# Performance work log

Measured on AMD Instinct MI355X. Metric: run time of the kernel, lower is better.

The kernel has to match this reference:

```python
import jax, jax.numpy as jnp
import numpy as np

B, H, W = 64, 512, 512


def setup_inputs() -> dict:
    key = jax.random.key(0)
    k1, k2 = jax.random.split(key)
    t1 = jax.random.normal(k1, (B, H, W), dtype=jnp.float32)
    t2 = jax.random.normal(k2, (B, H, W), dtype=jnp.float32)
    return {"t1": t1, "t2": t2}


def _wass_p2(a, b):
    # a, b: [H, W] -> flatten to empirical distributions of N values each
    av = a.reshape(-1)
    bv = b.reshape(-1)
    n = av.shape[0]
    a_sorted = jnp.sort(av)
    b_sorted = jnp.sort(bv)
    all_values = jnp.sort(jnp.concatenate([av, bv]))  # [2N]
    deltas = jnp.diff(all_values)                      # [2N-1]
    q = all_values[:-1]
    # right-side searchsorted == count of values <= q  (empirical CDF * N)
    i1 = jnp.searchsorted(a_sorted, q, side="right")
    i2 = jnp.searchsorted(b_sorted, q, side="right")
    c1 = i1.astype(jnp.float32) / n
    c2 = i2.astype(jnp.float32) / n
    # p = 2 branch of the original loss
    return jnp.sqrt(jnp.sum(jnp.square(c1 - c2) * deltas))


def reference(t1, t2):
    losses = jax.vmap(_wass_p2)(t1, t2)  # [B]
    return jnp.mean(losses)
```

## Files before the change

### kernel.cpp

```cpp
#include <hip/hip_runtime.h>
#include <stdint.h>

#define LOG_N   18
#define N_PER   262144
#define BATCHES 64
#define NBINS   4096
#define HALFB   2048
#define HTPB    256
#define SPLITS  16
#define CHUNK   (N_PER / SPLITS)
#define HWORDS  (NBINS / 2)
#define GTPB    512
#define BPT     (NBINS / GTPB)

__device__ __forceinline__ uint32_t f2k(float f) {
    uint32_t u = __float_as_uint(f);
    uint32_t m = (uint32_t)((int32_t)u >> 31) | 0x80000000u;
    return (u ^ m) >> 16;
}
__device__ __forceinline__ uint32_t comp(uint32_t k) {
    bool pos = (k >= 0x8000u);
    int  c   = pos ? ((int)k - 0xB900 + HALFB) : ((int)k - 0x3F00);
    int  lo  = pos ? HALFB : 0;
    int  hi  = lo + HALFB - 1;
    c = c < lo ? lo : c;
    c = c > hi ? hi : c;
    return (uint32_t)c;
}
__device__ __forceinline__ float binEdge(uint32_t c) {
    uint32_t k = (c < HALFB) ? (0x3F00u + c) : (0xB900u + (c - HALFB));
    uint32_t x = k << 16;
    uint32_t u = (x & 0x80000000u) ? (x ^ 0x80000000u) : ~x;
    return __uint_as_float(u);
}

__global__ __launch_bounds__(HTPB) void hist_kernel(
        const float* __restrict__ t1, const float* __restrict__ t2,
        uint32_t* __restrict__ slices) {
    __shared__ uint32_t h[NBINS];
    int tid  = threadIdx.x;
    int tile = blockIdx.x;
    int segL = tile / SPLITS;
    int part = tile % SPLITS;
    int bat  = segL >> 1;
    {
        uint4 z; z.x = z.y = z.z = z.w = 0u;
        uint4* h4 = (uint4*)h;
#pragma unroll
        for (int i = 0; i < 4; ++i) h4[tid + i * HTPB] = z;
    }
    __syncthreads();
    const float4* p = (const float4*)(((segL & 1) ? t2 : t1)
                      + ((size_t)bat << LOG_N) + (size_t)part * CHUNK);
    for (int k = 0; k < 4; ++k) {
        float4 v0 = p[tid + (4 * k + 0) * HTPB];
        float4 v1 = p[tid + (4 * k + 1) * HTPB];
        float4 v2 = p[tid + (4 * k + 2) * HTPB];
        float4 v3 = p[tid + (4 * k + 3) * HTPB];
        atomicAdd(&h[comp(f2k(v0.x))], 1u); atomicAdd(&h[comp(f2k(v0.y))], 1u);
        atomicAdd(&h[comp(f2k(v0.z))], 1u); atomicAdd(&h[comp(f2k(v0.w))], 1u);
        atomicAdd(&h[comp(f2k(v1.x))], 1u); atomicAdd(&h[comp(f2k(v1.y))], 1u);
        atomicAdd(&h[comp(f2k(v1.z))], 1u); atomicAdd(&h[comp(f2k(v1.w))], 1u);
        atomicAdd(&h[comp(f2k(v2.x))], 1u); atomicAdd(&h[comp(f2k(v2.y))], 1u);
        atomicAdd(&h[comp(f2k(v2.z))], 1u); atomicAdd(&h[comp(f2k(v2.w))], 1u);
        atomicAdd(&h[comp(f2k(v3.x))], 1u); atomicAdd(&h[comp(f2k(v3.y))], 1u);
        atomicAdd(&h[comp(f2k(v3.z))], 1u); atomicAdd(&h[comp(f2k(v3.w))], 1u);
    }
    __syncthreads();
    {
        const uint4* h4 = (const uint4*)h;
        uint4* gs4 = (uint4*)(slices + (size_t)tile * HWORDS);
#pragma unroll
        for (int i = tid; i < HWORDS / 4; i += HTPB) {
            uint4 a = h4[2 * i], b = h4[2 * i + 1];
            uint4 o;
            o.x = a.x | (a.y << 16);
            o.y = a.z | (a.w << 16);
            o.z = b.x | (b.y << 16);
            o.w = b.z | (b.w << 16);
            gs4[i] = o;
        }
    }
}

__global__ __launch_bounds__(GTPB) void integ_kernel(
        const uint32_t* __restrict__ slices, double* losses, int ignored) {
    __shared__ short sdiff[NBINS];
    __shared__ int sa[GTPB], sb[GTPB];
    __shared__ double red[GTPB];
    int bl  = blockIdx.x;
    int tid = threadIdx.x;
    const uint32_t* SA = slices + (size_t)(2 * bl) * SPLITS * HWORDS;
    const uint32_t* SB = SA + (size_t)SPLITS * HWORDS;

    for (int w = tid; w < HWORDS; w += GTPB) {
        int d0 = 0, d1 = 0;
#pragma unroll
        for (int s = 0; s < SPLITS; ++s) {
            uint32_t a = SA[s * HWORDS + w];
            uint32_t b = SB[s * HWORDS + w];
            d0 += (int)(a & 0xFFFFu) - (int)(b & 0xFFFFu);
            d1 += (int)(a >> 16)     - (int)(b >> 16);
        }
        sdiff[2 * w]     = (short)d0;
        sdiff[2 * w + 1] = (short)d1;
    }
    __syncthreads();

    int k0 = tid * BPT;
    int diffs[BPT];
    int s = 0;
#pragma unroll
    for (int k = 0; k < BPT; ++k) { int d = sdiff[k0 + k]; diffs[k] = d; s += d; }
    sa[tid] = s;
    __syncthreads();
    int* cur = sa; int* nxt = sb;
    for (int off = 1; off < GTPB; off <<= 1) {
        int v = cur[tid] + ((tid >= off) ? cur[tid - off] : 0);
        nxt[tid] = v;
        __syncthreads();
        int* tmp = cur; cur = nxt; nxt = tmp;
    }
    int D = tid ? cur[tid - 1] : 0;

    double acc = 0.0;
    float vprev = binEdge((uint32_t)k0);
#pragma unroll
    for (int k = 0; k < BPT; ++k) {
        D += diffs[k];
        float vnext = binEdge((uint32_t)(k0 + k + 1));
        if (D) { double dd = (double)D; acc += dd * dd * (double)(vnext - vprev); }
        vprev = vnext;
    }
    red[tid] = acc;
    __syncthreads();
    for (int off = GTPB / 2; off > 0; off >>= 1) {
        if (tid < off) red[tid] += red[tid + off];
        __syncthreads();
    }
    if (tid == 0) {
        const double inv = 1.0 / ((double)N_PER * (double)N_PER);
        losses[bl] = sqrt(red[0] * inv);
    }
}

__global__ void final_kernel(const double* losses, float* out) {
    int tid = threadIdx.x;
    double loss = losses[tid];
    for (int off = 32; off > 0; off >>= 1)
        loss += __shfl_down(loss, off);
    if (tid == 0) out[0] = (float)(loss / (double)BATCHES);
}

extern "C" void kernel_launch(void* const* d_in, const int* in_sizes, int n_in,
                              void* d_out, int out_size, void* d_ws, size_t ws_size,
                              hipStream_t stream) {
    const float* t1 = (const float*)d_in[0];
    const float* t2 = (const float*)d_in[1];
    float* out = (float*)d_out;

    char* ws = (char*)d_ws;
    double*   losses = (double*)ws;
    uint32_t* slices = (uint32_t*)(ws + 1024);
    size_t need = 1024 + (size_t)2 * BATCHES * SPLITS * HWORDS * 4;
    if (ws_size < need) return;

    hipLaunchKernelGGL(hist_kernel, dim3(2 * BATCHES * SPLITS), dim3(HTPB), 0, stream,
                       t1, t2, slices);
    hipLaunchKernelGGL(integ_kernel, dim3(BATCHES), dim3(GTPB), 0, stream,
                       slices, losses, 0);
    hipLaunchKernelGGL(final_kernel, dim3(1), dim3(BATCHES), 0, stream, losses, out);
}
```

Measured before the change: 37.03 us.

## Histogram t1 minus t2 into one signed shared histogram per block

Each histogram block now handles the same chunk of both t1 and t2 with 512 threads, adding +1 for t1 values and -1 for t2 values, so it stores one signed difference histogram instead of two separate ones. This halves the number of slices written and read, and the integration kernel sums the signed 16-bit slices with uint4 loads. The change relies on the per-chunk difference fitting in a signed 16-bit field. It also halves the grid size, which means fewer blocks to hide latency.

```diff
diff --git a/kernel.cpp b/kernel.cpp
--- a/kernel.cpp
+++ b/kernel.cpp
@@ -6,10 +6,10 @@
 #define BATCHES 64
 #define NBINS   4096
 #define HALFB   2048
-#define HTPB    256
+#define HTPB    512
 #define SPLITS  16
 #define CHUNK   (N_PER / SPLITS)
-#define HWORDS  (NBINS / 2)
+#define SLICEW  (NBINS / 2)
 #define GTPB    512
 #define BPT     (NBINS / GTPB)
 
@@ -40,70 +40,85 @@
     __shared__ uint32_t h[NBINS];
     int tid  = threadIdx.x;
     int tile = blockIdx.x;
-    int segL = tile / SPLITS;
+    int bat  = tile / SPLITS;
     int part = tile % SPLITS;
-    int bat  = segL >> 1;
     {
         uint4 z; z.x = z.y = z.z = z.w = 0u;
         uint4* h4 = (uint4*)h;
-#pragma unroll
-        for (int i = 0; i < 4; ++i) h4[tid + i * HTPB] = z;
+        h4[tid] = z; h4[tid + HTPB] = z;
     }
     __syncthreads();
-    const float4* p = (const float4*)(((segL & 1) ? t2 : t1)
-                      + ((size_t)bat << LOG_N) + (size_t)part * CHUNK);
-    for (int k = 0; k < 4; ++k) {
-        float4 v0 = p[tid + (4 * k + 0) * HTPB];
-        float4 v1 = p[tid + (4 * k + 1) * HTPB];
-        float4 v2 = p[tid + (4 * k + 2) * HTPB];
-        float4 v3 = p[tid + (4 * k + 3) * HTPB];
-        atomicAdd(&h[comp(f2k(v0.x))], 1u); atomicAdd(&h[comp(f2k(v0.y))], 1u);
-        atomicAdd(&h[comp(f2k(v0.z))], 1u); atomicAdd(&h[comp(f2k(v0.w))], 1u);
-        atomicAdd(&h[comp(f2k(v1.x))], 1u); atomicAdd(&h[comp(f2k(v1.y))], 1u);
-        atomicAdd(&h[comp(f2k(v1.z))], 1u); atomicAdd(&h[comp(f2k(v1.w))], 1u);
-        atomicAdd(&h[comp(f2k(v2.x))], 1u); atomicAdd(&h[comp(f2k(v2.y))], 1u);
-        atomicAdd(&h[comp(f2k(v2.z))], 1u); atomicAdd(&h[comp(f2k(v2.w))], 1u);
-        atomicAdd(&h[comp(f2k(v3.x))], 1u); atomicAdd(&h[comp(f2k(v3.y))], 1u);
-        atomicAdd(&h[comp(f2k(v3.z))], 1u); atomicAdd(&h[comp(f2k(v3.w))], 1u);
+    size_t boff = ((size_t)bat << LOG_N) + (size_t)part * CHUNK;
+    const float4* pA = (const float4*)(t1 + boff);
+    const float4* pB = (const float4*)(t2 + boff);
+#pragma unroll
+    for (int k = 0; k < 2; ++k) {
+        float4 a0 = pA[tid + (4 * k + 0) * HTPB];
+        float4 a1 = pA[tid + (4 * k + 1) * HTPB];
+        float4 a2 = pA[tid + (4 * k + 2) * HTPB];
+        float4 a3 = pA[tid + (4 * k + 3) * HTPB];
+        atomicAdd(&h[comp(f2k(a0.x))], 1u); atomicAdd(&h[comp(f2k(a0.y))], 1u);
+        atomicAdd(&h[comp(f2k(a0.z))], 1u); atomicAdd(&h[comp(f2k(a0.w))], 1u);
+        atomicAdd(&h[comp(f2k(a1.x))], 1u); atomicAdd(&h[comp(f2k(a1.y))], 1u);
+        atomicAdd(&h[comp(f2k(a1.z))], 1u); atomicAdd(&h[comp(f2k(a1.w))], 1u);
+        atomicAdd(&h[comp(f2k(a2.x))], 1u); atomicAdd(&h[comp(f2k(a2.y))], 1u);
+        atomicAdd(&h[comp(f2k(a2.z))], 1u); atomicAdd(&h[comp(f2k(a2.w))], 1u);
+        atomicAdd(&h[comp(f2k(a3.x))], 1u); atomicAdd(&h[comp(f2k(a3.y))], 1u);
+        atomicAdd(&h[comp(f2k(a3.z))], 1u); atomicAdd(&h[comp(f2k(a3.w))], 1u);
+    }
+#pragma unroll
+    for (int k = 0; k < 2; ++k) {
+        float4 b0 = pB[tid + (4 * k + 0) * HTPB];
+        float4 b1 = pB[tid + (4 * k + 1) * HTPB];
+        float4 b2 = pB[tid + (4 * k + 2) * HTPB];
+        float4 b3 = pB[tid + (4 * k + 3) * HTPB];
+        atomicAdd(&h[comp(f2k(b0.x))], (uint32_t)-1); atomicAdd(&h[comp(f2k(b0.y))], (uint32_t)-1);
+        atomicAdd(&h[comp(f2k(b0.z))], (uint32_t)-1); atomicAdd(&h[comp(f2k(b0.w))], (uint32_t)-1);
+        atomicAdd(&h[comp(f2k(b1.x))], (uint32_t)-1); atomicAdd(&h[comp(f2k(b1.y))], (uint32_t)-1);
+        atomicAdd(&h[comp(f2k(b1.z))], (uint32_t)-1); atomicAdd(&h[comp(f2k(b1.w))], (uint32_t)-1);
+        atomicAdd(&h[comp(f2k(b2.x))], (uint32_t)-1); atomicAdd(&h[comp(f2k(b2.y))], (uint32_t)-1);
+        atomicAdd(&h[comp(f2k(b2.z))], (uint32_t)-1); atomicAdd(&h[comp(f2k(b2.w))], (uint32_t)-1);
+        atomicAdd(&h[comp(f2k(b3.x))], (uint32_t)-1); atomicAdd(&h[comp(f2k(b3.y))], (uint32_t)-1);
+        atomicAdd(&h[comp(f2k(b3.z))], (uint32_t)-1); atomicAdd(&h[comp(f2k(b3.w))], (uint32_t)-1);
     }
     __syncthreads();
     {
         const uint4* h4 = (const uint4*)h;
-        uint4* gs4 = (uint4*)(slices + (size_t)tile * HWORDS);
-#pragma unroll
-        for (int i = tid; i < HWORDS / 4; i += HTPB) {
-            uint4 a = h4[2 * i], b = h4[2 * i + 1];
-            uint4 o;
-            o.x = a.x | (a.y << 16);
-            o.y = a.z | (a.w << 16);
-            o.z = b.x | (b.y << 16);
-            o.w = b.z | (b.w << 16);
-            gs4[i] = o;
-        }
+        uint4* gs4 = (uint4*)(slices + (size_t)tile * SLICEW);
+        uint4 a = h4[2 * tid], b = h4[2 * tid + 1];
+        uint4 o;
+        o.x = (a.x & 0xFFFFu) | (a.y << 16);
+        o.y = (a.z & 0xFFFFu) | (a.w << 16);
+        o.z = (b.x & 0xFFFFu) | (b.y << 16);
+        o.w = (b.z & 0xFFFFu) | (b.w << 16);
+        gs4[tid] = o;
     }
 }
 
 __global__ __launch_bounds__(GTPB) void integ_kernel(
-        const uint32_t* __restrict__ slices, double* losses, int ignored) {
+        const uint32_t* __restrict__ slices, double* losses) {
     __shared__ short sdiff[NBINS];
     __shared__ int sa[GTPB], sb[GTPB];
     __shared__ double red[GTPB];
     int bl  = blockIdx.x;
     int tid = threadIdx.x;
-    const uint32_t* SA = slices + (size_t)(2 * bl) * SPLITS * HWORDS;
-    const uint32_t* SB = SA + (size_t)SPLITS * HWORDS;
+    const uint4* S4 = (const uint4*)(slices + (size_t)bl * SPLITS * SLICEW);
+    const int W4 = SLICEW / 4;
 
-    for (int w = tid; w < HWORDS; w += GTPB) {
-        int d0 = 0, d1 = 0;
+    {
+        int d[8];
+#pragma unroll
+        for (int i = 0; i < 8; ++i) d[i] = 0;
 #pragma unroll
         for (int s = 0; s < SPLITS; ++s) {
-            uint32_t a = SA[s * HWORDS + w];
-            uint32_t b = SB[s * HWORDS + w];
-            d0 += (int)(a & 0xFFFFu) - (int)(b & 0xFFFFu);
-            d1 += (int)(a >> 16)     - (int)(b >> 16);
+            uint4 v = S4[s * W4 + tid];
+            d[0] += (int)(short)(v.x & 0xFFFFu); d[1] += (int)(short)(v.x >> 16);
+            d[2] += (int)(short)(v.y & 0xFFFFu); d[3] += (int)(short)(v.y >> 16);
+            d[4] += (int)(short)(v.z & 0xFFFFu); d[5] += (int)(short)(v.z >> 16);
+            d[6] += (int)(short)(v.w & 0xFFFFu); d[7] += (int)(short)(v.w >> 16);
         }
-        sdiff[2 * w]     = (short)d0;
-        sdiff[2 * w + 1] = (short)d1;
+#pragma unroll
+        for (int i = 0; i < 8; ++i) sdiff[8 * tid + i] = (short)d[i];
     }
     __syncthreads();
 
@@ -162,12 +177,12 @@
     char* ws = (char*)d_ws;
     double*   losses = (double*)ws;
     uint32_t* slices = (uint32_t*)(ws + 1024);
-    size_t need = 1024 + (size_t)2 * BATCHES * SPLITS * HWORDS * 4;
+    size_t need = 1024 + (size_t)BATCHES * SPLITS * SLICEW * 4;
     if (ws_size < need) return;
 
-    hipLaunchKernelGGL(hist_kernel, dim3(2 * BATCHES * SPLITS), dim3(HTPB), 0, stream,
+    hipLaunchKernelGGL(hist_kernel, dim3(BATCHES * SPLITS), dim3(HTPB), 0, stream,
                        t1, t2, slices);
     hipLaunchKernelGGL(integ_kernel, dim3(BATCHES), dim3(GTPB), 0, stream,
-                       slices, losses, 0);
+                       slices, losses);
     hipLaunchKernelGGL(final_kernel, dim3(1), dim3(BATCHES), 0, stream, losses, out);
 }
```

Result: faster. 32.88 us (-11.2%).
